# Kernel optimization log

Hardware: AMD Instinct MI355X
Metric: run time of the kernel (lower is better)

The kernel has to match this reference:

```python
import jax, jax.numpy as jnp
import numpy as np

E = 400000   # num edges / interactions
N = 50000    # num nodes
R = 6        # num_radial
H = 128      # hidden_channels
D = 256      # out_emb_channels
L = 3        # num_layers
O = 1        # out_channels


def setup_inputs() -> dict:
    key = jax.random.key(0)
    ks = jax.random.split(key, 8)
    x = jax.random.normal(ks[0], (E, H), dtype=jnp.float32)
    rbf = jax.random.uniform(ks[1], (E, R), dtype=jnp.float32)
    i = jax.random.randint(ks[2], (E,), 0, N)
    # learned params (glorot-ish scaling); Linear(in,out) stored as [in,out]
    w_rbf = jax.random.normal(ks[3], (R, H), dtype=jnp.float32) / np.float32(np.sqrt(R))
    w_up = jax.random.normal(ks[4], (H, D), dtype=jnp.float32) / np.float32(np.sqrt(H))
    Ws = jax.random.normal(ks[5], (L, D, D), dtype=jnp.float32) / np.float32(np.sqrt(D))
    bs = jnp.zeros((L, D), dtype=jnp.float32)
    w_out = jax.random.normal(ks[6], (D, O), dtype=jnp.float32) / np.float32(np.sqrt(D))
    return {"x": x, "rbf": rbf, "i": i, "w_rbf": w_rbf, "w_up": w_up,
            "Ws": Ws, "bs": bs, "w_out": w_out, "num_nodes": N}


def reference(x, rbf, i, w_rbf, w_up, Ws, bs, w_out, num_nodes):
    # elementwise scale: lin_rbf(rbf) * x   [E,H]
    h = (rbf @ w_rbf) * x
    # scatter-sum (segment reduce) over edge->node index   [N,H]
    x_spe = jax.ops.segment_sum(h, i, num_segments=num_nodes)
    # MLP tower (num_aux=0 -> single tower), applied to edge-level h as in source
    t = h @ w_up                      # [E,D]
    for l in range(Ws.shape[0]):
        t = jax.nn.silu(t @ Ws[l] + bs[l])
    out = t @ w_out                   # [E,O]
    return (x_spe, out)
```

## Files before the change

### kernel.cpp

```cpp
#include <hip/hip_runtime.h>

#define E_TOT   400000
#define N_NODES 50000
#define H_DIM   128
#define D_DIM   256
#define TE      128
#define NBLK    (E_TOT / TE)
#define NSCAN_BLK 196

typedef _Float16 f16x8 __attribute__((ext_vector_type(8)));
typedef float    f32x2 __attribute__((ext_vector_type(2)));
typedef float    f32x4 __attribute__((ext_vector_type(4)));
typedef float    f32x16 __attribute__((ext_vector_type(16)));

__device__ __forceinline__ int swz(int row, int col) {
    return row * 256 + (col ^ ((row & 7) << 3));
}

__device__ __forceinline__ f32x16 zero16() {
    f32x16 z = {0.f,0.f,0.f,0.f,0.f,0.f,0.f,0.f,0.f,0.f,0.f,0.f,0.f,0.f,0.f,0.f};
    return z;
}

__global__ void prep_weights(const float* __restrict__ w_up,
                             const float* __restrict__ Ws,
                             _Float16* __restrict__ wf)
{
    int t = blockIdx.x * 256 + threadIdx.x;
    int j    = t & 7;
    int lane = (t >> 3) & 63;
    int frag = t >> 9;
    int khalf = (lane >> 5) << 3;
    int col31 = lane & 31;
    float v;
    if (frag < 64) {
        int nb = frag >> 3, kb = frag & 7;
        v = w_up[(kb * 16 + khalf + j) * 256 + nb * 32 + col31];
    } else {
        int f2 = frag - 64;
        int layer = f2 >> 7;
        int fl = f2 & 127;
        int nb = fl >> 4, kb = fl & 15;
        v = Ws[layer * 65536 + (kb * 16 + khalf + j) * 256 + nb * 32 + col31];
    }
    wf[t] = (_Float16)v;
}

__global__ void k_hist(const int* __restrict__ ni, int* __restrict__ counts) {
    int e = blockIdx.x * 256 + threadIdx.x;
    if (e < E_TOT) atomicAdd(&counts[ni[e]], 1);
}

__global__ void k_scan_block(const int* __restrict__ counts,
                             int* __restrict__ starts, int* __restrict__ bsum) {
    __shared__ int s[256];
    int tid = threadIdx.x;
    int idx = blockIdx.x * 256 + tid;
    int v = (idx < N_NODES) ? counts[idx] : 0;
    s[tid] = v; __syncthreads();
    #pragma unroll
    for (int off = 1; off < 256; off <<= 1) {
        int t = (tid >= off) ? s[tid - off] : 0; __syncthreads();
        s[tid] += t; __syncthreads();
    }
    if (idx < N_NODES) starts[idx] = s[tid] - v;
    if (tid == 255) bsum[blockIdx.x] = s[255];
}

__global__ void k_scan_top(int* __restrict__ bsum) {
    __shared__ int s[256];
    int tid = threadIdx.x;
    int v = (tid < NSCAN_BLK) ? bsum[tid] : 0;
    s[tid] = v; __syncthreads();
    #pragma unroll
    for (int off = 1; off < 256; off <<= 1) {
        int t = (tid >= off) ? s[tid - off] : 0; __syncthreads();
        s[tid] += t; __syncthreads();
    }
    if (tid < NSCAN_BLK) bsum[tid] = s[tid] - v;
}

__global__ void k_scan_add(int* __restrict__ starts, const int* __restrict__ bsum,
                           int* __restrict__ cursor) {
    int idx = blockIdx.x * 256 + threadIdx.x;
    if (idx < N_NODES) {
        int v = starts[idx] + bsum[blockIdx.x];
        starts[idx] = v;
        cursor[idx] = v;
    }
    if (idx == 0) starts[N_NODES] = E_TOT;
}

__global__ void k_scatter(const int* __restrict__ ni, int* __restrict__ cursor,
                          int* __restrict__ eid) {
    int e = blockIdx.x * 256 + threadIdx.x;
    if (e < E_TOT) {
        int slot = atomicAdd(&cursor[ni[e]], 1);
        eid[slot] = e;
    }
}

__global__ __launch_bounds__(256)
void k_gather(const float* __restrict__ x, const float* __restrict__ rbf,
              const float* __restrict__ w_rbf, const int* __restrict__ starts,
              const int* __restrict__ eid, float* __restrict__ xspe)
{
    int wid  = threadIdx.x >> 6;
    int l    = threadIdx.x & 63;
    int node = blockIdx.x * 4 + wid;
    int c0   = l * 2;

    float wr[6][2];
    #pragma unroll
    for (int r = 0; r < 6; ++r) {
        wr[r][0] = w_rbf[r * 128 + c0];
        wr[r][1] = w_rbf[r * 128 + c0 + 1];
    }

    int kb = starts[node], ke = starts[node + 1];
    float a0 = 0.f, a1 = 0.f;
    for (int k = kb; k < ke; ++k) {
        int e = eid[k];
        float rb[6];
        #pragma unroll
        for (int r = 0; r < 6; ++r) rb[r] = rbf[(size_t)e * 6 + r];
        f32x2 xv = *(const f32x2*)(x + (size_t)e * 128 + c0);
        float s0 = 0.f, s1 = 0.f;
        #pragma unroll
        for (int r = 0; r < 6; ++r) { s0 += rb[r] * wr[r][0]; s1 += rb[r] * wr[r][1]; }
        a0 += s0 * xv[0];
        a1 += s1 * xv[1];
    }
    f32x2 o = {a0, a1};
    *(f32x2*)(xspe + (size_t)node * 128 + c0) = o;
}

__global__ __launch_bounds__(512, 4)
void fused_main(const float* __restrict__ x,
                const float* __restrict__ rbf,
                const float* __restrict__ w_rbf,
                const float* __restrict__ bs,
                const float* __restrict__ w_out,
                const _Float16* __restrict__ wf,
                float* __restrict__ out)
{
    __shared__ __align__(16) _Float16 tbuf[TE * 256];
    const int tid = threadIdx.x;
    const int e0  = blockIdx.x * TE;

    {
        const int cg = tid & 15;
        const int eg = tid >> 4;
        const int c0 = cg << 3;
        float wr[6][8];
        #pragma unroll
        for (int r = 0; r < 6; ++r)
            #pragma unroll
            for (int c = 0; c < 8; ++c)
                wr[r][c] = w_rbf[r * 128 + c0 + c];

        #pragma unroll
        for (int ee = 0; ee < 4; ++ee) {
            int el = eg * 4 + ee;
            int e  = e0 + el;
            float rb[6];
            #pragma unroll
            for (int r = 0; r < 6; ++r) rb[r] = rbf[(size_t)e * 6 + r];
            f32x4 xv0 = *(const f32x4*)(x + (size_t)e * 128 + c0);
            f32x4 xv1 = *(const f32x4*)(x + (size_t)e * 128 + c0 + 4);
            f16x8 hv;
            #pragma unroll
            for (int c = 0; c < 8; ++c) {
                float s = 0.f;
                #pragma unroll
                for (int r = 0; r < 6; ++r) s += rb[r] * wr[r][c];
                float xvv = (c < 4) ? xv0[c] : xv1[c - 4];
                hv[c] = (_Float16)(s * xvv);
            }
            *(f16x8*)&tbuf[swz(el, c0)] = hv;
        }
    }
    __syncthreads();

    const int l    = tid & 63;
    const int w    = tid >> 6;
    const int rs   = w >> 2;
    const int cs   = w & 3;
    const int l31  = l & 31;
    const int lh   = l >> 5;
    const int khalf = lh << 3;
    const int r0   = rs * 64;

    const f16x8* __restrict__ wupf = (const f16x8*)wf;
    const f16x8* __restrict__ wlf  = ((const f16x8*)wf) + 4096;

    f32x16 acc00, acc01, acc10, acc11;

    acc00 = acc01 = acc10 = acc11 = zero16();
    {
        f16x8 bc0 = wupf[((cs * 2 + 0) * 8 + 0) * 64 + l];
        f16x8 bc1 = wupf[((cs * 2 + 1) * 8 + 0) * 64 + l];
        #pragma unroll
        for (int kb = 0; kb < 8; ++kb) {
            f16x8 bn0, bn1;
            if (kb < 7) {
                bn0 = wupf[((cs * 2 + 0) * 8 + kb + 1) * 64 + l];
                bn1 = wupf[((cs * 2 + 1) * 8 + kb + 1) * 64 + l];
            }
            int k0 = kb * 16 + khalf;
            f16x8 a0 = *(const f16x8*)&tbuf[swz(r0 +  0 + l31, k0)];
            f16x8 a1 = *(const f16x8*)&tbuf[swz(r0 + 32 + l31, k0)];
            acc00 = __builtin_amdgcn_mfma_f32_32x32x16_f16(a0, bc0, acc00, 0, 0, 0);
            acc10 = __builtin_amdgcn_mfma_f32_32x32x16_f16(a1, bc0, acc10, 0, 0, 0);
            acc01 = __builtin_amdgcn_mfma_f32_32x32x16_f16(a0, bc1, acc01, 0, 0, 0);
            acc11 = __builtin_amdgcn_mfma_f32_32x32x16_f16(a1, bc1, acc11, 0, 0, 0);
            bc0 = bn0; bc1 = bn1;
        }
    }
    __syncthreads();
    {
        int cg0 = cs * 64 + l31;
        #pragma unroll
        for (int r = 0; r < 16; ++r) {
            int rowl = (r & 3) + 8 * (r >> 2) + 4 * lh;
            tbuf[swz(r0 +  0 + rowl, cg0)]      = (_Float16)acc00[r];
            tbuf[swz(r0 +  0 + rowl, cg0 + 32)] = (_Float16)acc01[r];
            tbuf[swz(r0 + 32 + rowl, cg0)]      = (_Float16)acc10[r];
            tbuf[swz(r0 + 32 + rowl, cg0 + 32)] = (_Float16)acc11[r];
        }
    }
    __syncthreads();

    for (int layer = 0; layer < 3; ++layer) {
        const f16x8* wl = wlf + layer * 8192;
        float bias0 = bs[layer * 256 + cs * 64 + l31];
        float bias1 = bs[layer * 256 + cs * 64 + 32 + l31];
        acc00 = acc01 = acc10 = acc11 = zero16();

        f16x8 bc0 = wl[((cs * 2 + 0) * 16 + 0) * 64 + l];
        f16x8 bc1 = wl[((cs * 2 + 1) * 16 + 0) * 64 + l];
        #pragma unroll
        for (int kb = 0; kb < 16; ++kb) {
            f16x8 bn0, bn1;
            if (kb < 15) {
                bn0 = wl[((cs * 2 + 0) * 16 + kb + 1) * 64 + l];
                bn1 = wl[((cs * 2 + 1) * 16 + kb + 1) * 64 + l];
            }
            int k0 = kb * 16 + khalf;
            f16x8 a0 = *(const f16x8*)&tbuf[swz(r0 +  0 + l31, k0)];
            f16x8 a1 = *(const f16x8*)&tbuf[swz(r0 + 32 + l31, k0)];
            acc00 = __builtin_amdgcn_mfma_f32_32x32x16_f16(a0, bc0, acc00, 0, 0, 0);
            acc10 = __builtin_amdgcn_mfma_f32_32x32x16_f16(a1, bc0, acc10, 0, 0, 0);
            acc01 = __builtin_amdgcn_mfma_f32_32x32x16_f16(a0, bc1, acc01, 0, 0, 0);
            acc11 = __builtin_amdgcn_mfma_f32_32x32x16_f16(a1, bc1, acc11, 0, 0, 0);
            bc0 = bn0; bc1 = bn1;
        }
        __syncthreads();
        {
            int cg0 = cs * 64 + l31;
            #pragma unroll
            for (int r = 0; r < 16; ++r) {
                int rowl = (r & 3) + 8 * (r >> 2) + 4 * lh;
                float v00 = acc00[r] + bias0;
                float v01 = acc01[r] + bias1;
                float v10 = acc10[r] + bias0;
                float v11 = acc11[r] + bias1;
                float s00 = __builtin_amdgcn_rcpf(1.0f + __expf(-v00));
                float s01 = __builtin_amdgcn_rcpf(1.0f + __expf(-v01));
                float s10 = __builtin_amdgcn_rcpf(1.0f + __expf(-v10));
                float s11 = __builtin_amdgcn_rcpf(1.0f + __expf(-v11));
                tbuf[swz(r0 +  0 + rowl, cg0)]      = (_Float16)(v00 * s00);
                tbuf[swz(r0 +  0 + rowl, cg0 + 32)] = (_Float16)(v01 * s01);
                tbuf[swz(r0 + 32 + rowl, cg0)]      = (_Float16)(v10 * s10);
                tbuf[swz(r0 + 32 + rowl, cg0 + 32)] = (_Float16)(v11 * s11);
            }
        }
        __syncthreads();
    }

    {
        int el = tid >> 2;
        int q  = tid & 3;
        int cbase = q * 64;
        float sum = 0.f;
        #pragma unroll
        for (int cc = 0; cc < 64; cc += 8) {
            int c = cbase + cc;
            f16x8 tv = *(const f16x8*)&tbuf[swz(el, c)];
            #pragma unroll
            for (int jj = 0; jj < 8; ++jj)
                sum += (float)tv[jj] * w_out[c + jj];
        }
        sum += __shfl_xor(sum, 1);
        sum += __shfl_xor(sum, 2);
        if (q == 0) out[e0 + el] = sum;
    }
}

extern "C" void kernel_launch(void* const* d_in, const int* in_sizes, int n_in,
                              void* d_out, int out_size, void* d_ws, size_t ws_size,
                              hipStream_t stream)
{
    const float* x     = (const float*)d_in[0];
    const float* rbf   = (const float*)d_in[1];
    const int*   nidx  = (const int*)d_in[2];
    const float* w_rbf = (const float*)d_in[3];
    const float* w_up  = (const float*)d_in[4];
    const float* Ws    = (const float*)d_in[5];
    const float* bs    = (const float*)d_in[6];
    const float* w_out = (const float*)d_in[7];

    float* xspe = (float*)d_out;
    float* outp = xspe + (size_t)N_NODES * H_DIM;

    char* ws = (char*)d_ws;
    _Float16* wf   = (_Float16*)ws;
    int* counts    = (int*)(ws + 0x080000);
    int* starts    = (int*)(ws + 0x0C0000);
    int* cursor    = (int*)(ws + 0x100000);
    int* bsum      = (int*)(ws + 0x140000);
    int* eid       = (int*)(ws + 0x150000);

    hipMemsetAsync(counts, 0, N_NODES * sizeof(int), stream);
    prep_weights<<<dim3(896), dim3(256), 0, stream>>>(w_up, Ws, wf);
    k_hist      <<<dim3(1563), dim3(256), 0, stream>>>(nidx, counts);
    k_scan_block<<<dim3(NSCAN_BLK), dim3(256), 0, stream>>>(counts, starts, bsum);
    k_scan_top  <<<dim3(1), dim3(256), 0, stream>>>(bsum);
    k_scan_add  <<<dim3(NSCAN_BLK), dim3(256), 0, stream>>>(starts, bsum, cursor);
    k_scatter   <<<dim3(1563), dim3(256), 0, stream>>>(nidx, cursor, eid);
    fused_main  <<<dim3(NBLK), dim3(512), 0, stream>>>(x, rbf, w_rbf, bs, w_out, wf, outp);
    k_gather    <<<dim3(12500), dim3(256), 0, stream>>>(x, rbf, w_rbf, starts, eid, xspe);
}
```

Before: 702.0 us.

## Fold node gather into fused MLP kernel via interleaved block roles

Merges the separate segment-sum gather kernel into the main MLP kernel. Every fifth block acts as a gather block, with each wave handling eight nodes, while the other blocks run the MLP tile. The aim is to overlap the memory-bound gather with the compute-bound MLP and remove one launch. It also changes the h-tile staging to 4-column chunks and staggers the output-dot LDS reads per quarter-wave to cut bank conflicts. The change leaves several dead no-op statements and may imbalance work, since the gather blocks hold LDS and registers sized for the MLP path.

```diff
diff --git a/kernel.cpp b/kernel.cpp
--- a/kernel.cpp
+++ b/kernel.cpp
@@ -6,8 +6,10 @@
 #define D_DIM   256
 #define TE      128
 #define NBLK    (E_TOT / TE)
+#define NB_TOT  3910
 #define NSCAN_BLK 196
 
+typedef _Float16 f16x4 __attribute__((ext_vector_type(4)));
 typedef _Float16 f16x8 __attribute__((ext_vector_type(8)));
 typedef float    f32x2 __attribute__((ext_vector_type(2)));
 typedef float    f32x4 __attribute__((ext_vector_type(4)));
@@ -100,41 +102,6 @@
     }
 }
 
-__global__ __launch_bounds__(256)
-void k_gather(const float* __restrict__ x, const float* __restrict__ rbf,
-              const float* __restrict__ w_rbf, const int* __restrict__ starts,
-              const int* __restrict__ eid, float* __restrict__ xspe)
-{
-    int wid  = threadIdx.x >> 6;
-    int l    = threadIdx.x & 63;
-    int node = blockIdx.x * 4 + wid;
-    int c0   = l * 2;
-
-    float wr[6][2];
-    #pragma unroll
-    for (int r = 0; r < 6; ++r) {
-        wr[r][0] = w_rbf[r * 128 + c0];
-        wr[r][1] = w_rbf[r * 128 + c0 + 1];
-    }
-
-    int kb = starts[node], ke = starts[node + 1];
-    float a0 = 0.f, a1 = 0.f;
-    for (int k = kb; k < ke; ++k) {
-        int e = eid[k];
-        float rb[6];
-        #pragma unroll
-        for (int r = 0; r < 6; ++r) rb[r] = rbf[(size_t)e * 6 + r];
-        f32x2 xv = *(const f32x2*)(x + (size_t)e * 128 + c0);
-        float s0 = 0.f, s1 = 0.f;
-        #pragma unroll
-        for (int r = 0; r < 6; ++r) { s0 += rb[r] * wr[r][0]; s1 += rb[r] * wr[r][1]; }
-        a0 += s0 * xv[0];
-        a1 += s1 * xv[1];
-    }
-    f32x2 o = {a0, a1};
-    *(f32x2*)(xspe + (size_t)node * 128 + c0) = o;
-}
-
 __global__ __launch_bounds__(512, 4)
 void fused_main(const float* __restrict__ x,
                 const float* __restrict__ rbf,
@@ -142,42 +109,97 @@
                 const float* __restrict__ bs,
                 const float* __restrict__ w_out,
                 const _Float16* __restrict__ wf,
+                const int* __restrict__ starts,
+                const int* __restrict__ eid,
+                float* __restrict__ xspe,
                 float* __restrict__ out)
 {
     __shared__ __align__(16) _Float16 tbuf[TE * 256];
     const int tid = threadIdx.x;
-    const int e0  = blockIdx.x * TE;
+    const int bid = blockIdx.x;
+
+    if ((bid % 5) == 4) {
+        int gbid = bid / 5;
+        int w    = tid >> 6;
+        int l    = tid & 63;
+        int node = gbid * 8 + w;
+        if (node >= N_NODES / 8) { }
+        node = gbid * 8 + w;
+        if (node < 6256) {
+            int nd = node * 8;
+        }
+        int n0 = gbid * 8 + w;
+        if (n0 < 50000 / 8 + 1) { }
+        int nodeid = gbid * 8 + w;
+        if (nodeid * 8 >= 0) { }
+        {
+            int nn = gbid * 8 + w;
+            if (nn < 6250 * 8) { }
+        }
+        int node_i = gbid * 8 + w;
+        int c0 = l * 2;
+        float wr[6][2];
+        #pragma unroll
+        for (int r = 0; r < 6; ++r) {
+            wr[r][0] = w_rbf[r * 128 + c0];
+            wr[r][1] = w_rbf[r * 128 + c0 + 1];
+        }
+        #pragma unroll
+        for (int rep = 0; rep < 8; ++rep) {
+            int nd = (gbid * 8 + w) * 8 + rep;
+            if (nd >= N_NODES) break;
+            int kb = starts[nd], ke = starts[nd + 1];
+            float a0 = 0.f, a1 = 0.f;
+            for (int k = kb; k < ke; ++k) {
+                int e = eid[k];
+                float rb[6];
+                #pragma unroll
+                for (int r = 0; r < 6; ++r) rb[r] = rbf[(size_t)e * 6 + r];
+                f32x2 xv = *(const f32x2*)(x + (size_t)e * 128 + c0);
+                float s0 = 0.f, s1 = 0.f;
+                #pragma unroll
+                for (int r = 0; r < 6; ++r) { s0 += rb[r] * wr[r][0]; s1 += rb[r] * wr[r][1]; }
+                a0 += s0 * xv[0];
+                a1 += s1 * xv[1];
+            }
+            f32x2 o = {a0, a1};
+            *(f32x2*)(xspe + (size_t)nd * 128 + c0) = o;
+        }
+        return;
+    }
+
+    const int tbid = bid - bid / 5;
+    if (tbid >= NBLK) return;
+    const int e0 = tbid * TE;
 
     {
-        const int cg = tid & 15;
-        const int eg = tid >> 4;
-        const int c0 = cg << 3;
-        float wr[6][8];
+        const int cg = tid & 31;
+        const int eg = tid >> 5;
+        const int c0 = cg << 2;
+        float wr[6][4];
         #pragma unroll
         for (int r = 0; r < 6; ++r)
             #pragma unroll
-            for (int c = 0; c < 8; ++c)
+            for (int c = 0; c < 4; ++c)
                 wr[r][c] = w_rbf[r * 128 + c0 + c];
 
         #pragma unroll
-        for (int ee = 0; ee < 4; ++ee) {
-            int el = eg * 4 + ee;
+        for (int ee = 0; ee < 8; ++ee) {
+            int el = eg * 8 + ee;
             int e  = e0 + el;
             float rb[6];
             #pragma unroll
             for (int r = 0; r < 6; ++r) rb[r] = rbf[(size_t)e * 6 + r];
-            f32x4 xv0 = *(const f32x4*)(x + (size_t)e * 128 + c0);
-            f32x4 xv1 = *(const f32x4*)(x + (size_t)e * 128 + c0 + 4);
-            f16x8 hv;
-            #pragma unroll
-            for (int c = 0; c < 8; ++c) {
+            f32x4 xv = *(const f32x4*)(x + (size_t)e * 128 + c0);
+            f16x4 hv;
+            #pragma unroll
+            for (int c = 0; c < 4; ++c) {
                 float s = 0.f;
                 #pragma unroll
                 for (int r = 0; r < 6; ++r) s += rb[r] * wr[r][c];
-                float xvv = (c < 4) ? xv0[c] : xv1[c - 4];
-                hv[c] = (_Float16)(s * xvv);
-            }
-            *(f16x8*)&tbuf[swz(el, c0)] = hv;
+                hv[c] = (_Float16)(s * xv[c]);
+            }
+            *(f16x4*)&tbuf[swz(el, c0)] = hv;
         }
     }
     __syncthreads();
@@ -284,8 +306,8 @@
         int cbase = q * 64;
         float sum = 0.f;
         #pragma unroll
-        for (int cc = 0; cc < 64; cc += 8) {
-            int c = cbase + cc;
+        for (int ch = 0; ch < 8; ++ch) {
+            int c = cbase + (((ch + q * 2) & 7) << 3);
             f16x8 tv = *(const f16x8*)&tbuf[swz(el, c)];
             #pragma unroll
             for (int jj = 0; jj < 8; ++jj)
@@ -328,6 +350,6 @@
     k_scan_top  <<<dim3(1), dim3(256), 0, stream>>>(bsum);
     k_scan_add  <<<dim3(NSCAN_BLK), dim3(256), 0, stream>>>(starts, bsum, cursor);
     k_scatter   <<<dim3(1563), dim3(256), 0, stream>>>(nidx, cursor, eid);
-    fused_main  <<<dim3(NBLK), dim3(512), 0, stream>>>(x, rbf, w_rbf, bs, w_out, wf, outp);
-    k_gather    <<<dim3(12500), dim3(256), 0, stream>>>(x, rbf, w_rbf, starts, eid, xspe);
-}
+    fused_main  <<<dim3(NB_TOT), dim3(512), 0, stream>>>(x, rbf, w_rbf, bs, w_out,
+                                                         wf, starts, eid, xspe, outp);
+}
```

Result: slower. 755.1 us (+7.6%).
